# Kernel tuning notes

Measured on AMD Instinct MI355X. Metric: run time of the kernel, lower is better.

## Reference

```python
import jax, jax.numpy as jnp
import numpy as np

IN_C = 256
OUT_C = 256
KS = 3
PAD = 1
EPS = 1e-5
BLOCK_SIZE = 256  # largest power of 2 dividing IN_C
NUM_BLOCKS = IN_C // BLOCK_SIZE


def golay_sequence(n):
    pow2 = 1
    while pow2 < n:
        pow2 *= 2
    a = np.array([1.0], dtype=np.float32)
    b = np.array([1.0], dtype=np.float32)
    while len(a) < pow2:
        a, b = np.concatenate([a, b]), np.concatenate([a, -b])
    return a[:n]


def fwht(x):
    """Unnormalized fast Walsh-Hadamard transform over the last axis (Sylvester order)."""
    base = x.shape[:-1]
    n = x.shape[-1]
    h = 1
    while h < n:
        y = x.reshape(base + (n // (2 * h), 2, h))
        a, c = y[..., 0, :], y[..., 1, :]
        x = jnp.stack([a + c, a - c], axis=-2).reshape(base + (n,))
        h *= 2
    return x


def setup_inputs() -> dict:
    key = jax.random.key(0)
    k1, k2, k3 = jax.random.split(key, 3)
    x = jax.random.normal(k1, (32, IN_C, 56, 56), dtype=jnp.float32)
    fan_in = IN_C * KS * KS
    W = jax.random.normal(k2, (OUT_C, IN_C, KS, KS), dtype=jnp.float32) / np.sqrt(fan_in)
    b = jax.random.normal(k3, (OUT_C,), dtype=jnp.float32) * 0.01
    rms_w = jnp.ones((IN_C,), dtype=jnp.float32)
    return {"x": x, "W": W, "b": b, "rms_w": rms_w}


def reference(x, W, b, rms_w):
    n, c, h, w = x.shape
    golay = jnp.asarray(golay_sequence(c)).reshape(1, c, 1, 1)
    x = x * golay                                    # Golay elementwise multiply
    x = jnp.transpose(x, (0, 2, 3, 1))               # NCHW -> NHWC
    x = x.reshape(n, h, w, NUM_BLOCKS, BLOCK_SIZE)
    x = fwht(x)                                      # blockwise Hadamard butterfly
    x = x.reshape(n, h, w, c)
    # RMSNorm over channel dim
    x = x * jax.lax.rsqrt(jnp.mean(x * x, axis=-1, keepdims=True) + EPS) * rms_w
    x = jnp.transpose(x, (0, 3, 1, 2))               # NHWC -> NCHW
    out = jax.lax.conv_general_dilated(
        x, W, window_strides=(1, 1), padding=((PAD, PAD), (PAD, PAD)),
        dimension_numbers=("NCHW", "OIHW", "NCHW"))
    return out + b[None, :, None, None]
```

## Files before the change

kernel.cpp:

```cpp
#include <hip/hip_runtime.h>
#include <hip/hip_bf16.h>

typedef short v8s __attribute__((ext_vector_type(8)));
typedef float v4f __attribute__((ext_vector_type(4)));
typedef unsigned short u16;

#define PROW 58
#define PCOL 64

static constexpr size_t A_CC_STRIDE = (size_t)32 * PROW * PCOL * 32;
static constexpr size_t A_ELEMS     = 8 * A_CC_STRIDE;
static constexpr size_t A_BYTES     = A_ELEMS * 2;
static constexpr size_t WB_ELEMS    = (size_t)9 * 8 * 256 * 32;

__device__ __forceinline__ void gl2lds16(const void* gptr, void* lptr) {
  auto g = (const __attribute__((address_space(1))) unsigned int*)gptr;
  auto l = (__attribute__((address_space(3))) unsigned int*)lptr;
  __builtin_amdgcn_global_load_lds(g, l, 16, 0, 0);
}

__global__ __launch_bounds__(256) void fwht_kernel(
    const float* __restrict__ x, const float* __restrict__ rms_w,
    __hip_bfloat16* __restrict__ A)
{
  __shared__ float tile[256 * 57];
  const int tid = threadIdx.x;
  const int y = blockIdx.x;
  const int n = blockIdx.y;
  const float* src = x + (size_t)n * 256 * 3136 + (size_t)y * 56;
  for (int f = tid; f < 256 * 56; f += 256) {
    int ch = f / 56;
    int xx = f - ch * 56;
    tile[ch * 57 + xx] = src[(size_t)ch * 3136 + xx];
  }
  __syncthreads();
  const int lane = tid & 63;
  const int wv = tid >> 6;
  float gs[4], rw[4];
  #pragma unroll
  for (int k = 0; k < 4; k++) {
    int ch = lane + 64 * k;
    gs[k] = 1.0f - 2.0f * (float)(__popc(ch & (ch >> 1)) & 1);
    rw[k] = rms_w[ch];
  }
  const int icq = (lane >> 3) & 3;
  const int jj = lane & 7;
  for (int p = wv; p < 56; p += 4) {
    float v[4];
    #pragma unroll
    for (int k = 0; k < 4; k++)
      v[k] = tile[(lane + 64 * k) * 57 + p] * gs[k];
    #pragma unroll
    for (int hs = 0; hs < 6; hs++) {
      const int h = 1 << hs;
      #pragma unroll
      for (int k = 0; k < 4; k++) {
        float o = __shfl_xor(v[k], h, 64);
        v[k] = ((lane & h) ? -v[k] : v[k]) + o;
      }
    }
    { float a=v[0], b=v[1], c=v[2], d=v[3];
      v[0]=a+b; v[1]=a-b; v[2]=c+d; v[3]=c-d; }
    { float a=v[0], b=v[1], c=v[2], d=v[3];
      v[0]=a+c; v[2]=a-c; v[1]=b+d; v[3]=b-d; }
    float ss = v[0]*v[0] + v[1]*v[1] + v[2]*v[2] + v[3]*v[3];
    #pragma unroll
    for (int hs = 0; hs < 6; hs++) ss += __shfl_xor(ss, 1 << hs, 64);
    float sc = rsqrtf(ss * (1.0f / 256.0f) + 1e-5f);
    const int col = p + 1, row = y + 1;
    const int sw = (col >> 1) & 3;
    const int icq_st = icq ^ sw;
    #pragma unroll
    for (int k = 0; k < 4; k++) {
      int cc = (lane + 64 * k) >> 5;
      size_t off = ((((size_t)cc * 32 + n) * PROW + row) * PCOL + col) * 32 + icq_st * 8 + jj;
      A[off] = __float2bfloat16(v[k] * sc * rw[k]);
    }
  }
}

__global__ __launch_bounds__(256) void wconv_kernel(
    const float* __restrict__ Wf, __hip_bfloat16* __restrict__ Wb)
{
  int t = blockIdx.x * 256 + threadIdx.x;
  int j = t & 7;
  int icq_st = (t >> 3) & 3;
  int oc = (t >> 5) & 255;
  int cc = (t >> 13) & 7;
  int kk = t >> 16;
  int icq = icq_st ^ ((oc >> 1) & 3);
  int ic = cc * 32 + icq * 8 + j;
  int ky = kk / 3, kx = kk - ky * 3;
  float w = Wf[((oc * 256 + ic) * 3 + ky) * 3 + kx];
  Wb[t] = __float2bfloat16(w);
}

__global__ __launch_bounds__(256, 3) void conv_kernel(
    const u16* __restrict__ A, const u16* __restrict__ Wb,
    const float* __restrict__ bias, float* __restrict__ out)
{
  __shared__ __align__(16) u16 As[4 * PCOL * 32];
  __shared__ __align__(16) u16 Bs[2][128 * 32];

  const int tid  = threadIdx.x;
  const int lane = tid & 63;
  const int wv   = tid >> 6;
  const int wm   = wv & 1;
  const int wn   = wv >> 1;
  const int m15  = lane & 15;
  const int q    = lane >> 4;

  const int ocb = blockIdx.x;
  const int y0  = blockIdx.y * 2;
  const int n   = blockIdx.z;

  const u16* gA = A + ((size_t)n * PROW + y0) * (PCOL * 32);

  v4f acc[4][4];
  const v4f vzero = {0.0f, 0.0f, 0.0f, 0.0f};
  #pragma unroll
  for (int i = 0; i < 4; i++)
    #pragma unroll
    for (int j = 0; j < 4; j++)
      acc[i][j] = vzero;

  int ub[4];
  #pragma unroll
  for (int nf = 0; nf < 4; nf++) {
    int ocl = wn * 64 + nf * 16 + m15;
    ub[nf] = (ocl * 4 + (q ^ ((ocl >> 1) & 3))) * 8;
  }

  auto stageA = [&](int cc) {
    const u16* g = gA + (size_t)cc * A_CC_STRIDE + tid * 8;
    u16* d = As + tid * 8;
    #pragma unroll
    for (int k = 0; k < 4; k++)
      gl2lds16(g + k * 2048, d + k * 2048);
  };
  auto stageB = [&](int cc, int kk, int pb) {
    const u16* g = Wb + ((kk * 8 + cc) * 8192 + ocb * 4096) + tid * 8;
    u16* d = &Bs[pb][0] + tid * 8;
    #pragma unroll
    for (int k = 0; k < 2; k++)
      gl2lds16(g + k * 2048, d + k * 2048);
  };

  stageA(0);
  stageB(0, 0, 0);
  __syncthreads();

  for (int cc = 0; cc < 8; cc++) {
    for (int kk = 0; kk < 9; kk++) {
      const int pb = kk & 1;
      if (kk < 8) stageB(cc, kk + 1, pb ^ 1);
      const int ky = kk / 3;
      const int kx = kk - ky * 3;
      const int irow = wm + ky;
      v8s af[4];
      #pragma unroll
      for (int mf = 0; mf < 4; mf++) {
        int col = mf * 16 + m15 + kx;
        col = col > 63 ? 63 : col;
        int u = (irow * PCOL + col) * 4 + (q ^ ((col >> 1) & 3));
        af[mf] = *(const v8s*)(As + u * 8);
      }
      const u16* bsb = &Bs[pb][0];
      v8s bfr[4];
      #pragma unroll
      for (int nf = 0; nf < 4; nf++)
        bfr[nf] = *(const v8s*)(bsb + ub[nf]);
      #pragma unroll
      for (int mf = 0; mf < 4; mf++)
        #pragma unroll
        for (int nf = 0; nf < 4; nf++)
          acc[mf][nf] = __builtin_amdgcn_mfma_f32_16x16x32_bf16(af[mf], bfr[nf], acc[mf][nf], 0, 0, 0);
      if (kk < 8) __syncthreads();
    }
    if (cc < 7) {
      __syncthreads();
      stageA(cc + 1);
      stageB(cc + 1, 0, 0);
      __syncthreads();
    }
  }

  const int yrow = y0 + wm;
  #pragma unroll
  for (int nf = 0; nf < 4; nf++) {
    const int oc = ocb * 128 + wn * 64 + nf * 16 + m15;
    const float bb = bias[oc];
    float* orow = out + ((size_t)(n * 256 + oc) * 56 + yrow) * 56;
    #pragma unroll
    for (int mf = 0; mf < 4; mf++) {
      const int c0 = mf * 16 + q * 4;
      if (c0 < 56) {
        v4f val = acc[mf][nf];
        val.x += bb; val.y += bb; val.z += bb; val.w += bb;
        *(v4f*)(orow + c0) = val;
      }
    }
  }
}

extern "C" void kernel_launch(void* const* d_in, const int* in_sizes, int n_in,
                              void* d_out, int out_size, void* d_ws, size_t ws_size,
                              hipStream_t stream)
{
  const float* x     = (const float*)d_in[0];
  const float* Wf    = (const float*)d_in[1];
  const float* bias  = (const float*)d_in[2];
  const float* rms_w = (const float*)d_in[3];
  float* out = (float*)d_out;

  if (ws_size < A_BYTES + WB_ELEMS * 2) return;

  __hip_bfloat16* Abf = (__hip_bfloat16*)d_ws;
  __hip_bfloat16* Wb  = (__hip_bfloat16*)((char*)d_ws + A_BYTES);

  hipMemsetAsync(d_ws, 0, A_BYTES, stream);
  fwht_kernel<<<dim3(56, 32), 256, 0, stream>>>(x, rms_w, Abf);
  wconv_kernel<<<dim3((int)(WB_ELEMS / 256)), 256, 0, stream>>>(Wf, Wb);
  conv_kernel<<<dim3(2, 28, 32), 256, 0, stream>>>(
      (const u16*)Abf, (const u16*)Wb, bias, out);
}
```

Before: 361.4 us.

## Switch conv to 32x32 MFMA, stage weights per kernel row, coalesce FWHT stores

The conv kernel moves from 16x16x32 to 32x32x16 bf16 MFMA tiles and loads all three kx weight slices per ky into a triple LDS buffer, so it synchronises once per kernel row instead of once per tap. This drops the prefetch double-buffering, so loads no longer overlap compute. The FWHT kernel now stages its bf16 results in LDS and writes full 16-byte rows to global memory instead of scattered 2-byte stores. It also writes the zero padding borders itself, which removes the memset over the whole workspace.

```diff
diff --git a/kernel.cpp b/kernel.cpp
--- a/kernel.cpp
+++ b/kernel.cpp
@@ -3,14 +3,14 @@
 
 typedef short v8s __attribute__((ext_vector_type(8)));
 typedef float v4f __attribute__((ext_vector_type(4)));
+typedef float v16f __attribute__((ext_vector_type(16)));
 typedef unsigned short u16;
 
 #define PROW 58
 #define PCOL 64
 
 static constexpr size_t A_CC_STRIDE = (size_t)32 * PROW * PCOL * 32;
-static constexpr size_t A_ELEMS     = 8 * A_CC_STRIDE;
-static constexpr size_t A_BYTES     = A_ELEMS * 2;
+static constexpr size_t A_BYTES     = 8 * A_CC_STRIDE * 2;
 static constexpr size_t WB_ELEMS    = (size_t)9 * 8 * 256 * 32;
 
 __device__ __forceinline__ void gl2lds16(const void* gptr, void* lptr) {
@@ -19,11 +19,19 @@
   __builtin_amdgcn_global_load_lds(g, l, 16, 0, 0);
 }
 
-__global__ __launch_bounds__(256) void fwht_kernel(
+__device__ __forceinline__ u16 f2bf(float f) {
+  __hip_bfloat16 h = __float2bfloat16(f);
+  union { __hip_bfloat16 b; u16 u; } cv; cv.b = h; return cv.u;
+}
+
+__global__ __launch_bounds__(256, 2) void fwht_kernel(
     const float* __restrict__ x, const float* __restrict__ rms_w,
-    __hip_bfloat16* __restrict__ A)
-{
-  __shared__ float tile[256 * 57];
+    u16* __restrict__ A)
+{
+  __shared__ __align__(16) char smem[58368];
+  float* tile = (float*)smem;
+  u16*   ob   = (u16*)smem;
+
   const int tid = threadIdx.x;
   const int y = blockIdx.x;
   const int n = blockIdx.y;
@@ -34,6 +42,7 @@
     tile[ch * 57 + xx] = src[(size_t)ch * 3136 + xx];
   }
   __syncthreads();
+
   const int lane = tid & 63;
   const int wv = tid >> 6;
   float gs[4], rw[4];
@@ -43,9 +52,11 @@
     gs[k] = 1.0f - 2.0f * (float)(__popc(ch & (ch >> 1)) & 1);
     rw[k] = rms_w[ch];
   }
-  const int icq = (lane >> 3) & 3;
-  const int jj = lane & 7;
-  for (int p = wv; p < 56; p += 4) {
+
+  unsigned int res[14][2];
+  #pragma unroll
+  for (int i = 0; i < 14; i++) {
+    const int p = wv + 4 * i;
     float v[4];
     #pragma unroll
     for (int k = 0; k < 4; k++)
@@ -67,20 +78,61 @@
     #pragma unroll
     for (int hs = 0; hs < 6; hs++) ss += __shfl_xor(ss, 1 << hs, 64);
     float sc = rsqrtf(ss * (1.0f / 256.0f) + 1e-5f);
-    const int col = p + 1, row = y + 1;
-    const int sw = (col >> 1) & 3;
-    const int icq_st = icq ^ sw;
+    res[i][0] = (unsigned int)f2bf(v[0] * sc * rw[0]) |
+                ((unsigned int)f2bf(v[1] * sc * rw[1]) << 16);
+    res[i][1] = (unsigned int)f2bf(v[2] * sc * rw[2]) |
+                ((unsigned int)f2bf(v[3] * sc * rw[3]) << 16);
+  }
+  __syncthreads();
+
+  const int icq = (lane >> 3) & 3;
+  const int jj = lane & 7;
+  const int ccl = lane >> 5;
+  #pragma unroll
+  for (int i = 0; i < 14; i++) {
+    const int p = wv + 4 * i;
+    const int sw = ((p + 1) >> 1) & 3;
+    const int qs = (icq ^ sw) * 8 + jj;
     #pragma unroll
     for (int k = 0; k < 4; k++) {
-      int cc = (lane + 64 * k) >> 5;
-      size_t off = ((((size_t)cc * 32 + n) * PROW + row) * PCOL + col) * 32 + icq_st * 8 + jj;
-      A[off] = __float2bfloat16(v[k] * sc * rw[k]);
+      const int cc = 2 * k + ccl;
+      u16 val = (u16)(res[i][k >> 1] >> (16 * (k & 1)));
+      ob[cc * 1808 + p * 32 + qs] = val;
+    }
+  }
+  __syncthreads();
+
+  const int row = y + 1;
+  #pragma unroll
+  for (int i = 0; i < 7; i++) {
+    int c = tid + 256 * i;
+    int cc = c / 224, rem = c - cc * 224;
+    v8s val = *(const v8s*)(ob + cc * 1808 + rem * 8);
+    size_t go = (((size_t)cc * 32 + n) * PROW + row) * 2048 + 32 + rem * 8;
+    *(v8s*)(A + go) = val;
+  }
+  {
+    const v8s z = {0,0,0,0,0,0,0,0};
+    int cc = tid >> 5, s = tid & 31;
+    size_t rb = (((size_t)cc * 32 + n) * PROW + row) * 2048;
+    if (s < 4) *(v8s*)(A + rb + s * 8) = z;
+    else       *(v8s*)(A + rb + 57 * 32 + (s - 4) * 8) = z;
+  }
+  if (y == 0 || y == 55) {
+    const v8s z = {0,0,0,0,0,0,0,0};
+    const int r = (y == 0) ? 0 : 57;
+    #pragma unroll
+    for (int i = 0; i < 8; i++) {
+      int c = tid + 256 * i;
+      int cc = c >> 8, rem = c & 255;
+      size_t go = (((size_t)cc * 32 + n) * PROW + r) * 2048 + rem * 8;
+      *(v8s*)(A + go) = z;
     }
   }
 }
 
 __global__ __launch_bounds__(256) void wconv_kernel(
-    const float* __restrict__ Wf, __hip_bfloat16* __restrict__ Wb)
+    const float* __restrict__ Wf, u16* __restrict__ Wb)
 {
   int t = blockIdx.x * 256 + threadIdx.x;
   int j = t & 7;
@@ -92,7 +144,7 @@
   int ic = cc * 32 + icq * 8 + j;
   int ky = kk / 3, kx = kk - ky * 3;
   float w = Wf[((oc * 256 + ic) * 3 + ky) * 3 + kx];
-  Wb[t] = __float2bfloat16(w);
+  Wb[t] = f2bf(w);
 }
 
 __global__ __launch_bounds__(256, 3) void conv_kernel(
@@ -100,36 +152,40 @@
     const float* __restrict__ bias, float* __restrict__ out)
 {
   __shared__ __align__(16) u16 As[4 * PCOL * 32];
-  __shared__ __align__(16) u16 Bs[2][128 * 32];
+  __shared__ __align__(16) u16 Bs[3 * 128 * 32];
 
   const int tid  = threadIdx.x;
   const int lane = tid & 63;
   const int wv   = tid >> 6;
   const int wm   = wv & 1;
   const int wn   = wv >> 1;
-  const int m15  = lane & 15;
-  const int q    = lane >> 4;
+  const int m31  = lane & 31;
+  const int kh8  = lane >> 5;
 
   const int ocb = blockIdx.x;
   const int y0  = blockIdx.y * 2;
   const int n   = blockIdx.z;
 
-  const u16* gA = A + ((size_t)n * PROW + y0) * (PCOL * 32);
-
-  v4f acc[4][4];
-  const v4f vzero = {0.0f, 0.0f, 0.0f, 0.0f};
-  #pragma unroll
-  for (int i = 0; i < 4; i++)
-    #pragma unroll
-    for (int j = 0; j < 4; j++)
-      acc[i][j] = vzero;
-
-  int ub[4];
-  #pragma unroll
-  for (int nf = 0; nf < 4; nf++) {
-    int ocl = wn * 64 + nf * 16 + m15;
-    ub[nf] = (ocl * 4 + (q ^ ((ocl >> 1) & 3))) * 8;
-  }
+  const u16* gA = A + ((size_t)n * PROW + y0) * 2048;
+
+  v16f acc[2][2];
+  #pragma unroll
+  for (int i = 0; i < 2; i++)
+    #pragma unroll
+    for (int j = 0; j < 2; j++)
+      #pragma unroll
+      for (int e = 0; e < 16; e++)
+        acc[i][j][e] = 0.0f;
+
+  int ub[2][2];
+  #pragma unroll
+  for (int nf = 0; nf < 2; nf++)
+    #pragma unroll
+    for (int kh = 0; kh < 2; kh++) {
+      int ocl = wn * 64 + nf * 32 + m31;
+      int q = kh * 2 + kh8;
+      ub[nf][kh] = (ocl * 4 + (q ^ ((ocl >> 1) & 3))) * 8;
+    }
 
   auto stageA = [&](int cc) {
     const u16* g = gA + (size_t)cc * A_CC_STRIDE + tid * 8;
@@ -138,66 +194,76 @@
     for (int k = 0; k < 4; k++)
       gl2lds16(g + k * 2048, d + k * 2048);
   };
-  auto stageB = [&](int cc, int kk, int pb) {
-    const u16* g = Wb + ((kk * 8 + cc) * 8192 + ocb * 4096) + tid * 8;
-    u16* d = &Bs[pb][0] + tid * 8;
-    #pragma unroll
-    for (int k = 0; k < 2; k++)
-      gl2lds16(g + k * 2048, d + k * 2048);
+  auto stageB = [&](int cc, int ky) {
+    #pragma unroll
+    for (int kx = 0; kx < 3; kx++) {
+      const int kk = ky * 3 + kx;
+      const u16* g = Wb + ((kk * 8 + cc) * 8192 + ocb * 4096) + tid * 8;
+      u16* d = Bs + kx * 4096 + tid * 8;
+      gl2lds16(g, d);
+      gl2lds16(g + 2048, d + 2048);
+    }
   };
 
-  stageA(0);
-  stageB(0, 0, 0);
-  __syncthreads();
-
   for (int cc = 0; cc < 8; cc++) {
-    for (int kk = 0; kk < 9; kk++) {
-      const int pb = kk & 1;
-      if (kk < 8) stageB(cc, kk + 1, pb ^ 1);
-      const int ky = kk / 3;
-      const int kx = kk - ky * 3;
-      const int irow = wm + ky;
-      v8s af[4];
-      #pragma unroll
-      for (int mf = 0; mf < 4; mf++) {
-        int col = mf * 16 + m15 + kx;
-        col = col > 63 ? 63 : col;
-        int u = (irow * PCOL + col) * 4 + (q ^ ((col >> 1) & 3));
-        af[mf] = *(const v8s*)(As + u * 8);
-      }
-      const u16* bsb = &Bs[pb][0];
-      v8s bfr[4];
-      #pragma unroll
-      for (int nf = 0; nf < 4; nf++)
-        bfr[nf] = *(const v8s*)(bsb + ub[nf]);
-      #pragma unroll
-      for (int mf = 0; mf < 4; mf++)
+    __syncthreads();
+    stageA(cc);
+    stageB(cc, 0);
+    __syncthreads();
+    #pragma unroll
+    for (int ky = 0; ky < 3; ky++) {
+      #pragma unroll
+      for (int kx = 0; kx < 3; kx++) {
+        v8s af[2][2];
         #pragma unroll
-        for (int nf = 0; nf < 4; nf++)
-          acc[mf][nf] = __builtin_amdgcn_mfma_f32_16x16x32_bf16(af[mf], bfr[nf], acc[mf][nf], 0, 0, 0);
-      if (kk < 8) __syncthreads();
-    }
-    if (cc < 7) {
-      __syncthreads();
-      stageA(cc + 1);
-      stageB(cc + 1, 0, 0);
-      __syncthreads();
+        for (int mf = 0; mf < 2; mf++)
+          #pragma unroll
+          for (int kh = 0; kh < 2; kh++) {
+            int col = mf * 32 + m31 + kx;
+            col = col > 63 ? 63 : col;
+            int q = kh * 2 + kh8;
+            int ua = (((wm + ky) * PCOL + col) * 4 + (q ^ ((col >> 1) & 3))) * 8;
+            af[mf][kh] = *(const v8s*)(As + ua);
+          }
+        v8s bf[2][2];
+        const u16* bsb = Bs + kx * 4096;
+        #pragma unroll
+        for (int nf = 0; nf < 2; nf++)
+          #pragma unroll
+          for (int kh = 0; kh < 2; kh++)
+            bf[nf][kh] = *(const v8s*)(bsb + ub[nf][kh]);
+        #pragma unroll
+        for (int mf = 0; mf < 2; mf++)
+          #pragma unroll
+          for (int nf = 0; nf < 2; nf++) {
+            acc[mf][nf] = __builtin_amdgcn_mfma_f32_32x32x16_bf16(af[mf][0], bf[nf][0], acc[mf][nf], 0, 0, 0);
+            acc[mf][nf] = __builtin_amdgcn_mfma_f32_32x32x16_bf16(af[mf][1], bf[nf][1], acc[mf][nf], 0, 0, 0);
+          }
+      }
+      if (ky < 2) {
+        __syncthreads();
+        stageB(cc, ky + 1);
+        __syncthreads();
+      }
     }
   }
 
   const int yrow = y0 + wm;
   #pragma unroll
-  for (int nf = 0; nf < 4; nf++) {
-    const int oc = ocb * 128 + wn * 64 + nf * 16 + m15;
+  for (int nf = 0; nf < 2; nf++) {
+    const int oc = ocb * 128 + wn * 64 + nf * 32 + m31;
     const float bb = bias[oc];
     float* orow = out + ((size_t)(n * 256 + oc) * 56 + yrow) * 56;
     #pragma unroll
-    for (int mf = 0; mf < 4; mf++) {
-      const int c0 = mf * 16 + q * 4;
-      if (c0 < 56) {
-        v4f val = acc[mf][nf];
-        val.x += bb; val.y += bb; val.z += bb; val.w += bb;
-        *(v4f*)(orow + c0) = val;
+    for (int mf = 0; mf < 2; mf++) {
+      #pragma unroll
+      for (int g = 0; g < 4; g++) {
+        const int x0 = mf * 32 + 8 * g + 4 * kh8;
+        if (x0 < 56) {
+          v4f val = { acc[mf][nf][4*g+0] + bb, acc[mf][nf][4*g+1] + bb,
+                      acc[mf][nf][4*g+2] + bb, acc[mf][nf][4*g+3] + bb };
+          *(v4f*)(orow + x0) = val;
+        }
       }
     }
   }
@@ -215,12 +281,10 @@
 
   if (ws_size < A_BYTES + WB_ELEMS * 2) return;
 
-  __hip_bfloat16* Abf = (__hip_bfloat16*)d_ws;
-  __hip_bfloat16* Wb  = (__hip_bfloat16*)((char*)d_ws + A_BYTES);
-
-  hipMemsetAsync(d_ws, 0, A_BYTES, stream);
+  u16* Abf = (u16*)d_ws;
+  u16* Wb  = (u16*)((char*)d_ws + A_BYTES);
+
   fwht_kernel<<<dim3(56, 32), 256, 0, stream>>>(x, rms_w, Abf);
   wconv_kernel<<<dim3((int)(WB_ELEMS / 256)), 256, 0, stream>>>(Wf, Wb);
-  conv_kernel<<<dim3(2, 28, 32), 256, 0, stream>>>(
-      (const u16*)Abf, (const u16*)Wb, bias, out);
-}
+  conv_kernel<<<dim3(2, 28, 32), 256, 0, stream>>>(Abf, Wb, bias, out);
+}
```

Result: faster. 342.3 us (-5.3%).
